# Optimization experiments

Measured on AMD Instinct MI355X. Metric: run time of the kernel, lower is better.

The kernel has to match this reference:

```python
import jax, jax.numpy as jnp
import numpy as np

HIDDEN = 512
KEY_DIM = HIDDEN // 8  # 64
B, N, M = 8, 2048, 2048


def setup_inputs() -> dict:
    key = jax.random.key(0)
    kx, ky, kwq, kbq, kwk, kbk = jax.random.split(key, 6)
    s = 1.0 / np.sqrt(HIDDEN)
    return {
        "x": jax.random.normal(kx, (B, N, HIDDEN), dtype=jnp.float32),
        "y": jax.random.normal(ky, (B, M, HIDDEN), dtype=jnp.float32),
        "Wq": jax.random.uniform(kwq, (KEY_DIM, HIDDEN), minval=-s, maxval=s, dtype=jnp.float32),
        "bq": jax.random.uniform(kbq, (KEY_DIM,), minval=-s, maxval=s, dtype=jnp.float32),
        "Wk": jax.random.uniform(kwk, (KEY_DIM, HIDDEN), minval=-s, maxval=s, dtype=jnp.float32),
        "bk": jax.random.uniform(kbk, (KEY_DIM,), minval=-s, maxval=s, dtype=jnp.float32),
    }


def reference(x, y, Wq, bq, Wk, bk):
    # linear projections (torch Linear: x @ W^T + b)
    q = jnp.einsum("bnh,kh->bnk", x, Wq) + bq  # [B,N,K]
    k = jnp.einsum("bmh,kh->bmk", y, Wk) + bk  # [B,M,K]
    # pairwise squared distance [B,N,M]
    dist = (
        -2.0 * jnp.einsum("bnk,bmk->bnm", q, k)
        + jnp.sum(q * q, axis=-1)[:, :, None]
        + jnp.sum(k * k, axis=-1)[:, None, :]
    )
    # max over M of exp(-dist), keepdim -> [B,N,1]
    atweight = jnp.max(jnp.exp(-dist), axis=-1, keepdims=True)
    # outer product per batch -> [B,N,N]
    attention = jnp.einsum("bni,bmi->bnm", atweight, atweight)
    return attention
```

## Files before the change

### kernel.cpp

```cpp
#include <hip/hip_runtime.h>

#define B_   8
#define N_   2048
#define H_   512
#define K_   64
#define NROWS 16384

__global__ __launch_bounds__(256) void proj_kernel(
    const float* __restrict__ x, const float* __restrict__ y,
    const float* __restrict__ Wq, const float* __restrict__ bq,
    const float* __restrict__ Wk, const float* __restrict__ bk,
    float* __restrict__ qout, float* __restrict__ kout,
    unsigned int* __restrict__ minT)
{
    __shared__ float Xs[64][68];
    __shared__ float Ws[64][68];

    const int tid = threadIdx.x;
    const int blk = blockIdx.x;
    const bool isQ = blk < (NROWS / 64);
    const float* __restrict__ X    = isQ ? x  : y;
    const float* __restrict__ W    = isQ ? Wq : Wk;
    const float* __restrict__ bias = isQ ? bq : bk;
    float* __restrict__ out        = isQ ? qout : kout;
    const int row0 = (isQ ? blk : blk - (NROWS / 64)) * 64;

    const int fid = blk * 256 + tid;
    if (fid < NROWS) minT[fid] = 0x7f800000u;

    const int lc = tid & 15;
    const int lr = tid >> 4;
    const int tx = tid & 15;
    const int ty = tid >> 4;

    float acc[4][4] = {};

    for (int c = 0; c < 8; ++c) {
        const int h0 = c * 64;
        #pragma unroll
        for (int p = 0; p < 4; ++p) {
            const int r = p * 16 + lr;
            const float4 v = *reinterpret_cast<const float4*>(
                &X[(size_t)(row0 + r) * H_ + h0 + lc * 4]);
            Xs[lc * 4 + 0][r] = v.x; Xs[lc * 4 + 1][r] = v.y;
            Xs[lc * 4 + 2][r] = v.z; Xs[lc * 4 + 3][r] = v.w;
        }
        #pragma unroll
        for (int p = 0; p < 4; ++p) {
            const int r = p * 16 + lr;
            const float4 v = *reinterpret_cast<const float4*>(
                &W[(size_t)r * H_ + h0 + lc * 4]);
            Ws[lc * 4 + 0][r] = v.x; Ws[lc * 4 + 1][r] = v.y;
            Ws[lc * 4 + 2][r] = v.z; Ws[lc * 4 + 3][r] = v.w;
        }
        __syncthreads();
        #pragma unroll 16
        for (int h = 0; h < 64; ++h) {
            const float4 xa = *reinterpret_cast<const float4*>(&Xs[h][ty * 4]);
            const float4 wb = *reinterpret_cast<const float4*>(&Ws[h][tx * 4]);
            const float xs[4] = {xa.x, xa.y, xa.z, xa.w};
            const float wsv[4] = {wb.x, wb.y, wb.z, wb.w};
            #pragma unroll
            for (int i = 0; i < 4; ++i)
                #pragma unroll
                for (int j = 0; j < 4; ++j)
                    acc[i][j] = fmaf(xs[i], wsv[j], acc[i][j]);
        }
        __syncthreads();
    }

    const float4 bf = *reinterpret_cast<const float4*>(&bias[tx * 4]);
    #pragma unroll
    for (int i = 0; i < 4; ++i) {
        float4 v;
        v.x = acc[i][0] + bf.x; v.y = acc[i][1] + bf.y;
        v.z = acc[i][2] + bf.z; v.w = acc[i][3] + bf.w;
        *reinterpret_cast<float4*>(
            &out[(size_t)(row0 + ty * 4 + i) * K_ + tx * 4]) = v;
    }
}

__global__ __launch_bounds__(256) void dist_kernel(
    const float* __restrict__ q, const float* __restrict__ kmat,
    unsigned int* __restrict__ minT)
{
    __shared__ float Qs[64][68];
    __shared__ float Ks[64][68];
    __shared__ float qqS[64], kkS[64];
    __shared__ float red[64][17];

    const int tid  = threadIdx.x;
    const int b    = blockIdx.z;
    const int nbase = blockIdx.y * 64;
    const int mbase = blockIdx.x * 64;
    const int lc = tid & 15, lr = tid >> 4;

    #pragma unroll
    for (int p = 0; p < 4; ++p) {
        const int r = p * 16 + lr;
        const float4 v = *reinterpret_cast<const float4*>(
            &q[(size_t)(b * N_ + nbase + r) * K_ + lc * 4]);
        Qs[lc * 4 + 0][r] = v.x; Qs[lc * 4 + 1][r] = v.y;
        Qs[lc * 4 + 2][r] = v.z; Qs[lc * 4 + 3][r] = v.w;
        const float4 u = *reinterpret_cast<const float4*>(
            &kmat[(size_t)(b * N_ + mbase + r) * K_ + lc * 4]);
        Ks[lc * 4 + 0][r] = u.x; Ks[lc * 4 + 1][r] = u.y;
        Ks[lc * 4 + 2][r] = u.z; Ks[lc * 4 + 3][r] = u.w;
    }
    __syncthreads();

    if (tid < 64) {
        float s = 0.f;
        #pragma unroll 8
        for (int h = 0; h < 64; ++h) s = fmaf(Qs[h][tid], Qs[h][tid], s);
        qqS[tid] = s;
    } else if (tid < 128) {
        const int t = tid - 64;
        float s = 0.f;
        #pragma unroll 8
        for (int h = 0; h < 64; ++h) s = fmaf(Ks[h][t], Ks[h][t], s);
        kkS[t] = s;
    }
    __syncthreads();

    const int tx = tid & 15;
    const int ty = tid >> 4;
    float acc[4][4] = {};
    #pragma unroll 16
    for (int h = 0; h < 64; ++h) {
        const float4 qa = *reinterpret_cast<const float4*>(&Qs[h][ty * 4]);
        const float4 kb = *reinterpret_cast<const float4*>(&Ks[h][tx * 4]);
        const float qs[4] = {qa.x, qa.y, qa.z, qa.w};
        const float ks[4] = {kb.x, kb.y, kb.z, kb.w};
        #pragma unroll
        for (int i = 0; i < 4; ++i)
            #pragma unroll
            for (int j = 0; j < 4; ++j)
                acc[i][j] = fmaf(qs[i], ks[j], acc[i][j]);
    }

    #pragma unroll
    for (int i = 0; i < 4; ++i) {
        const float qq = qqS[ty * 4 + i];
        float best = 1e30f;
        #pragma unroll
        for (int j = 0; j < 4; ++j) {
            const float d = qq + kkS[tx * 4 + j] - 2.0f * acc[i][j];
            best = fminf(best, d);
        }
        red[ty * 4 + i][tx] = best;
    }
    __syncthreads();

    if (tid < 64) {
        float best = red[tid][0];
        #pragma unroll
        for (int j = 1; j < 16; ++j) best = fminf(best, red[tid][j]);
        atomicMin(&minT[b * N_ + nbase + tid], __float_as_uint(best));
    }
}

__global__ __launch_bounds__(256) void wexp_kernel(
    const unsigned int* __restrict__ minT, float* __restrict__ w)
{
    const int i = blockIdx.x * 256 + threadIdx.x;
    if (i < NROWS) w[i] = expf(-__uint_as_float(minT[i]));
}

__global__ __launch_bounds__(256) void outer_kernel(
    const float* __restrict__ w, float4* __restrict__ out)
{
    const int f = blockIdx.x * 256 + threadIdx.x;
    const int m4 = f & 511;
    const int n  = (f >> 9) & 2047;
    const int b  = f >> 20;
    const float wn = w[(b << 11) + n];
    const float4 wm = reinterpret_cast<const float4*>(w)[(b << 9) + m4];
    float4 o;
    o.x = wn * wm.x; o.y = wn * wm.y; o.z = wn * wm.z; o.w = wn * wm.w;
    out[f] = o;
}

extern "C" void kernel_launch(void* const* d_in, const int* in_sizes, int n_in,
                              void* d_out, int out_size, void* d_ws, size_t ws_size,
                              hipStream_t stream)
{
    const float* x  = (const float*)d_in[0];
    const float* y  = (const float*)d_in[1];
    const float* Wq = (const float*)d_in[2];
    const float* bq = (const float*)d_in[3];
    const float* Wk = (const float*)d_in[4];
    const float* bk = (const float*)d_in[5];
    float* out = (float*)d_out;

    float* ws = (float*)d_ws;
    float* q = ws;
    float* k = ws + 1048576;
    unsigned int* minT = (unsigned int*)(ws + 2097152);
    float* w = ws + 2097152 + 16384;

    proj_kernel<<<512, 256, 0, stream>>>(x, y, Wq, bq, Wk, bk, q, k, minT);
    dist_kernel<<<dim3(32, 32, 8), 256, 0, stream>>>(q, k, minT);
    wexp_kernel<<<64, 256, 0, stream>>>(minT, w);
    outer_kernel<<<32768, 256, 0, stream>>>(w, (float4*)out);
}
```

Before: 294.7 us.

## Use split-bf16 MFMA for projection and distance, fuse min and exp

Both the projection GEMM and the pairwise distance GEMM move from scalar FP32 FMA to bf16 MFMA. To keep accuracy near FP32, each operand is split into high and low bf16 parts and three MFMA products are summed. The distance kernel now has each wave keep a running minimum over all M keys in registers, then applies exp itself. This removes the atomicMin pass, the minT init and the separate exp kernel. The costs are a small weight-conversion kernel, triple MFMA work, and a possible precision risk from the bf16x3 approximation.

```diff
diff --git a/kernel.cpp b/kernel.cpp
--- a/kernel.cpp
+++ b/kernel.cpp
@@ -1,170 +1,194 @@
 #include <hip/hip_runtime.h>
 
-#define B_   8
-#define N_   2048
-#define H_   512
-#define K_   64
+#define B_    8
+#define N_    2048
+#define H_    512
+#define K_    64
 #define NROWS 16384
-
-__global__ __launch_bounds__(256) void proj_kernel(
+#define RTOT  32768
+
+typedef __attribute__((ext_vector_type(8))) __bf16 bf16x8;
+typedef __attribute__((ext_vector_type(4))) float  floatx4;
+
+#define MFMA(a, b, c) __builtin_amdgcn_mfma_f32_16x16x32_bf16((a), (b), (c), 0, 0, 0)
+
+__global__ __launch_bounds__(256) void wcvt_kernel(
+    const float* __restrict__ Wq, const float* __restrict__ Wk,
+    __bf16* __restrict__ Whilo)
+{
+    const int i = blockIdx.x * 256 + threadIdx.x;
+    const bool isQ = i < 32768;
+    const int off = isQ ? i : i - 32768;
+    const float f = isQ ? Wq[off] : Wk[off];
+    const __bf16 h = (__bf16)f;
+    const __bf16 l = (__bf16)(f - (float)h);
+    const int base = isQ ? 0 : 65536;
+    Whilo[base + off] = h;
+    Whilo[base + 32768 + off] = l;
+}
+
+__global__ __launch_bounds__(128) void proj_kernel(
     const float* __restrict__ x, const float* __restrict__ y,
-    const float* __restrict__ Wq, const float* __restrict__ bq,
-    const float* __restrict__ Wk, const float* __restrict__ bk,
-    float* __restrict__ qout, float* __restrict__ kout,
-    unsigned int* __restrict__ minT)
-{
-    __shared__ float Xs[64][68];
-    __shared__ float Ws[64][68];
-
-    const int tid = threadIdx.x;
-    const int blk = blockIdx.x;
-    const bool isQ = blk < (NROWS / 64);
-    const float* __restrict__ X    = isQ ? x  : y;
-    const float* __restrict__ W    = isQ ? Wq : Wk;
+    const __bf16* __restrict__ Whilo,
+    const float* __restrict__ bq, const float* __restrict__ bk,
+    __bf16* __restrict__ qh, __bf16* __restrict__ ql,
+    float* __restrict__ sq)
+{
+    const int tid  = threadIdx.x;
+    const int wv   = tid >> 6;
+    const int lane = tid & 63;
+    const int quad = lane >> 4;
+    const int l16  = lane & 15;
+    const int rowbase = blockIdx.x * 64 + wv * 32;
+    const bool isQ = rowbase < NROWS;
+    const float* __restrict__ X   = isQ ? x : y;
+    const int xrow0 = isQ ? rowbase : rowbase - NROWS;
+    const __bf16* __restrict__ Whi = Whilo + (isQ ? 0 : 2 * 32768);
+    const __bf16* __restrict__ Wlo = Whi + 32768;
     const float* __restrict__ bias = isQ ? bq : bk;
-    float* __restrict__ out        = isQ ? qout : kout;
-    const int row0 = (isQ ? blk : blk - (NROWS / 64)) * 64;
-
-    const int fid = blk * 256 + tid;
-    if (fid < NROWS) minT[fid] = 0x7f800000u;
-
-    const int lc = tid & 15;
-    const int lr = tid >> 4;
-    const int tx = tid & 15;
-    const int ty = tid >> 4;
-
-    float acc[4][4] = {};
-
-    for (int c = 0; c < 8; ++c) {
-        const int h0 = c * 64;
-        #pragma unroll
-        for (int p = 0; p < 4; ++p) {
-            const int r = p * 16 + lr;
-            const float4 v = *reinterpret_cast<const float4*>(
-                &X[(size_t)(row0 + r) * H_ + h0 + lc * 4]);
-            Xs[lc * 4 + 0][r] = v.x; Xs[lc * 4 + 1][r] = v.y;
-            Xs[lc * 4 + 2][r] = v.z; Xs[lc * 4 + 3][r] = v.w;
-        }
-        #pragma unroll
-        for (int p = 0; p < 4; ++p) {
-            const int r = p * 16 + lr;
-            const float4 v = *reinterpret_cast<const float4*>(
-                &W[(size_t)r * H_ + h0 + lc * 4]);
-            Ws[lc * 4 + 0][r] = v.x; Ws[lc * 4 + 1][r] = v.y;
-            Ws[lc * 4 + 2][r] = v.z; Ws[lc * 4 + 3][r] = v.w;
-        }
-        __syncthreads();
-        #pragma unroll 16
-        for (int h = 0; h < 64; ++h) {
-            const float4 xa = *reinterpret_cast<const float4*>(&Xs[h][ty * 4]);
-            const float4 wb = *reinterpret_cast<const float4*>(&Ws[h][tx * 4]);
-            const float xs[4] = {xa.x, xa.y, xa.z, xa.w};
-            const float wsv[4] = {wb.x, wb.y, wb.z, wb.w};
-            #pragma unroll
-            for (int i = 0; i < 4; ++i)
-                #pragma unroll
-                for (int j = 0; j < 4; ++j)
-                    acc[i][j] = fmaf(xs[i], wsv[j], acc[i][j]);
-        }
-        __syncthreads();
-    }
-
-    const float4 bf = *reinterpret_cast<const float4*>(&bias[tx * 4]);
-    #pragma unroll
-    for (int i = 0; i < 4; ++i) {
-        float4 v;
-        v.x = acc[i][0] + bf.x; v.y = acc[i][1] + bf.y;
-        v.z = acc[i][2] + bf.z; v.w = acc[i][3] + bf.w;
-        *reinterpret_cast<float4*>(
-            &out[(size_t)(row0 + ty * 4 + i) * K_ + tx * 4]) = v;
-    }
-}
-
-__global__ __launch_bounds__(256) void dist_kernel(
-    const float* __restrict__ q, const float* __restrict__ kmat,
-    unsigned int* __restrict__ minT)
-{
-    __shared__ float Qs[64][68];
-    __shared__ float Ks[64][68];
-    __shared__ float qqS[64], kkS[64];
-    __shared__ float red[64][17];
-
+
+    floatx4 acc[2][4];
+    #pragma unroll
+    for (int rt = 0; rt < 2; ++rt)
+        #pragma unroll
+        for (int ot = 0; ot < 4; ++ot)
+            acc[rt][ot] = floatx4{0.f, 0.f, 0.f, 0.f};
+
+    for (int it = 0; it < 16; ++it) {
+        const int k0 = it * 32 + quad * 8;
+        bf16x8 ahi[2], alo[2];
+        #pragma unroll
+        for (int rt = 0; rt < 2; ++rt) {
+            const float4 f0 = *reinterpret_cast<const float4*>(
+                &X[(size_t)(xrow0 + rt * 16 + l16) * H_ + k0]);
+            const float4 f1 = *reinterpret_cast<const float4*>(
+                &X[(size_t)(xrow0 + rt * 16 + l16) * H_ + k0 + 4]);
+            const float fv[8] = {f0.x, f0.y, f0.z, f0.w, f1.x, f1.y, f1.z, f1.w};
+            #pragma unroll
+            for (int j = 0; j < 8; ++j) {
+                const __bf16 h = (__bf16)fv[j];
+                ahi[rt][j] = h;
+                alo[rt][j] = (__bf16)(fv[j] - (float)h);
+            }
+        }
+        bf16x8 bhi[4], blo[4];
+        #pragma unroll
+        for (int ot = 0; ot < 4; ++ot) {
+            const int wrow = ot * 16 + l16;
+            bhi[ot] = *reinterpret_cast<const bf16x8*>(&Whi[(size_t)wrow * H_ + k0]);
+            blo[ot] = *reinterpret_cast<const bf16x8*>(&Wlo[(size_t)wrow * H_ + k0]);
+        }
+        #pragma unroll
+        for (int rt = 0; rt < 2; ++rt)
+            #pragma unroll
+            for (int ot = 0; ot < 4; ++ot) {
+                acc[rt][ot] = MFMA(ahi[rt], bhi[ot], acc[rt][ot]);
+                acc[rt][ot] = MFMA(ahi[rt], blo[ot], acc[rt][ot]);
+                acc[rt][ot] = MFMA(alo[rt], bhi[ot], acc[rt][ot]);
+            }
+    }
+
+    float bv[4];
+    #pragma unroll
+    for (int ot = 0; ot < 4; ++ot) bv[ot] = bias[ot * 16 + l16];
+
+    #pragma unroll
+    for (int rt = 0; rt < 2; ++rt) {
+        float ss[4] = {0.f, 0.f, 0.f, 0.f};
+        #pragma unroll
+        for (int ot = 0; ot < 4; ++ot)
+            #pragma unroll
+            for (int r = 0; r < 4; ++r) {
+                const float qv = acc[rt][ot][r] + bv[ot];
+                acc[rt][ot][r] = qv;
+                ss[r] = fmaf(qv, qv, ss[r]);
+            }
+        #pragma unroll
+        for (int off = 1; off < 16; off <<= 1)
+            #pragma unroll
+            for (int r = 0; r < 4; ++r)
+                ss[r] += __shfl_xor(ss[r], off);
+        const int row0 = rowbase + rt * 16 + quad * 4;
+        if (l16 == 0) {
+            #pragma unroll
+            for (int r = 0; r < 4; ++r) sq[row0 + r] = ss[r];
+        }
+        #pragma unroll
+        for (int ot = 0; ot < 4; ++ot)
+            #pragma unroll
+            for (int r = 0; r < 4; ++r) {
+                const size_t idx = (size_t)(row0 + r) * K_ + ot * 16 + l16;
+                const float qv = acc[rt][ot][r];
+                const __bf16 h = (__bf16)qv;
+                qh[idx] = h;
+                ql[idx] = (__bf16)(qv - (float)h);
+            }
+    }
+}
+
+__global__ __launch_bounds__(128) void dist_kernel(
+    const __bf16* __restrict__ qh, const __bf16* __restrict__ ql,
+    const float* __restrict__ sq, float* __restrict__ wout)
+{
     const int tid  = threadIdx.x;
-    const int b    = blockIdx.z;
-    const int nbase = blockIdx.y * 64;
-    const int mbase = blockIdx.x * 64;
-    const int lc = tid & 15, lr = tid >> 4;
-
-    #pragma unroll
-    for (int p = 0; p < 4; ++p) {
-        const int r = p * 16 + lr;
-        const float4 v = *reinterpret_cast<const float4*>(
-            &q[(size_t)(b * N_ + nbase + r) * K_ + lc * 4]);
-        Qs[lc * 4 + 0][r] = v.x; Qs[lc * 4 + 1][r] = v.y;
-        Qs[lc * 4 + 2][r] = v.z; Qs[lc * 4 + 3][r] = v.w;
-        const float4 u = *reinterpret_cast<const float4*>(
-            &kmat[(size_t)(b * N_ + mbase + r) * K_ + lc * 4]);
-        Ks[lc * 4 + 0][r] = u.x; Ks[lc * 4 + 1][r] = u.y;
-        Ks[lc * 4 + 2][r] = u.z; Ks[lc * 4 + 3][r] = u.w;
-    }
-    __syncthreads();
-
-    if (tid < 64) {
-        float s = 0.f;
-        #pragma unroll 8
-        for (int h = 0; h < 64; ++h) s = fmaf(Qs[h][tid], Qs[h][tid], s);
-        qqS[tid] = s;
-    } else if (tid < 128) {
-        const int t = tid - 64;
-        float s = 0.f;
-        #pragma unroll 8
-        for (int h = 0; h < 64; ++h) s = fmaf(Ks[h][t], Ks[h][t], s);
-        kkS[t] = s;
-    }
-    __syncthreads();
-
-    const int tx = tid & 15;
-    const int ty = tid >> 4;
-    float acc[4][4] = {};
-    #pragma unroll 16
-    for (int h = 0; h < 64; ++h) {
-        const float4 qa = *reinterpret_cast<const float4*>(&Qs[h][ty * 4]);
-        const float4 kb = *reinterpret_cast<const float4*>(&Ks[h][tx * 4]);
-        const float qs[4] = {qa.x, qa.y, qa.z, qa.w};
-        const float ks[4] = {kb.x, kb.y, kb.z, kb.w};
-        #pragma unroll
-        for (int i = 0; i < 4; ++i)
-            #pragma unroll
-            for (int j = 0; j < 4; ++j)
-                acc[i][j] = fmaf(qs[i], ks[j], acc[i][j]);
-    }
-
-    #pragma unroll
-    for (int i = 0; i < 4; ++i) {
-        const float qq = qqS[ty * 4 + i];
-        float best = 1e30f;
-        #pragma unroll
-        for (int j = 0; j < 4; ++j) {
-            const float d = qq + kkS[tx * 4 + j] - 2.0f * acc[i][j];
-            best = fminf(best, d);
-        }
-        red[ty * 4 + i][tx] = best;
-    }
-    __syncthreads();
-
-    if (tid < 64) {
-        float best = red[tid][0];
-        #pragma unroll
-        for (int j = 1; j < 16; ++j) best = fminf(best, red[tid][j]);
-        atomicMin(&minT[b * N_ + nbase + tid], __float_as_uint(best));
-    }
-}
-
-__global__ __launch_bounds__(256) void wexp_kernel(
-    const unsigned int* __restrict__ minT, float* __restrict__ w)
-{
-    const int i = blockIdx.x * 256 + threadIdx.x;
-    if (i < NROWS) w[i] = expf(-__uint_as_float(minT[i]));
+    const int wv   = tid >> 6;
+    const int lane = tid & 63;
+    const int quad = lane >> 4;
+    const int l16  = lane & 15;
+    const int blk  = blockIdx.x;
+    const int b    = blk >> 6;
+    const int nrow = (blk & 63) * 32 + wv * 16;
+    const size_t qrow = (size_t)(b * N_ + nrow + l16);
+
+    const bf16x8 ahi0 = *reinterpret_cast<const bf16x8*>(&qh[qrow * K_ + quad * 8]);
+    const bf16x8 ahi1 = *reinterpret_cast<const bf16x8*>(&qh[qrow * K_ + 32 + quad * 8]);
+    const bf16x8 alo0 = *reinterpret_cast<const bf16x8*>(&ql[qrow * K_ + quad * 8]);
+    const bf16x8 alo1 = *reinterpret_cast<const bf16x8*>(&ql[qrow * K_ + 32 + quad * 8]);
+
+    const __bf16* __restrict__ kh = qh + (size_t)NROWS * K_;
+    const __bf16* __restrict__ kl = ql + (size_t)NROWS * K_;
+    const float*  __restrict__ kk = sq + NROWS;
+
+    floatx4 runmin = floatx4{1e30f, 1e30f, 1e30f, 1e30f};
+
+    #pragma unroll 2
+    for (int ms = 0; ms < 128; ++ms) {
+        const size_t krow = (size_t)(b * N_ + ms * 16 + l16);
+        const bf16x8 bh0 = *reinterpret_cast<const bf16x8*>(&kh[krow * K_ + quad * 8]);
+        const bf16x8 bh1 = *reinterpret_cast<const bf16x8*>(&kh[krow * K_ + 32 + quad * 8]);
+        const bf16x8 bl0 = *reinterpret_cast<const bf16x8*>(&kl[krow * K_ + quad * 8]);
+        const bf16x8 bl1 = *reinterpret_cast<const bf16x8*>(&kl[krow * K_ + 32 + quad * 8]);
+        const float kkv = kk[b * N_ + ms * 16 + l16];
+
+        floatx4 acc = floatx4{0.f, 0.f, 0.f, 0.f};
+        acc = MFMA(ahi0, bh0, acc);
+        acc = MFMA(ahi1, bh1, acc);
+        acc = MFMA(ahi0, bl0, acc);
+        acc = MFMA(ahi1, bl1, acc);
+        acc = MFMA(alo0, bh0, acc);
+        acc = MFMA(alo1, bh1, acc);
+
+        #pragma unroll
+        for (int r = 0; r < 4; ++r) {
+            const float d = fmaf(-2.f, acc[r], kkv);
+            runmin[r] = fminf(runmin[r], d);
+        }
+    }
+
+    #pragma unroll
+    for (int off = 1; off < 16; off <<= 1)
+        #pragma unroll
+        for (int r = 0; r < 4; ++r)
+            runmin[r] = fminf(runmin[r], __shfl_xor(runmin[r], off));
+
+    if (l16 == 0) {
+        #pragma unroll
+        for (int r = 0; r < 4; ++r) {
+            const int row = nrow + quad * 4 + r;
+            const float d = runmin[r] + sq[b * N_ + row];
+            wout[b * N_ + row] = expf(-d);
+        }
+    }
 }
 
 __global__ __launch_bounds__(256) void outer_kernel(
@@ -193,14 +217,15 @@
     const float* bk = (const float*)d_in[5];
     float* out = (float*)d_out;
 
-    float* ws = (float*)d_ws;
-    float* q = ws;
-    float* k = ws + 1048576;
-    unsigned int* minT = (unsigned int*)(ws + 2097152);
-    float* w = ws + 2097152 + 16384;
-
-    proj_kernel<<<512, 256, 0, stream>>>(x, y, Wq, bq, Wk, bk, q, k, minT);
-    dist_kernel<<<dim3(32, 32, 8), 256, 0, stream>>>(q, k, minT);
-    wexp_kernel<<<64, 256, 0, stream>>>(minT, w);
+    char* ws = (char*)d_ws;
+    __bf16* qh    = (__bf16*)ws;
+    __bf16* ql    = (__bf16*)(ws + 4194304);
+    float*  sq    = (float*)(ws + 8388608);
+    __bf16* Whilo = (__bf16*)(ws + 8519680);
+    float*  w     = (float*)(ws + 8781824);
+
+    wcvt_kernel<<<256, 256, 0, stream>>>(Wq, Wk, Whilo);
+    proj_kernel<<<512, 128, 0, stream>>>(x, y, Whilo, bq, bk, qh, ql, sq);
+    dist_kernel<<<512, 128, 0, stream>>>(qh, ql, sq, w);
     outer_kernel<<<32768, 256, 0, stream>>>(w, (float4*)out);
 }
```

After: 262.6 us. 10.9% less time.
